# Optimization experiments

Hardware: AMD Instinct MI355X
Metric: run time of the kernel (lower is better)

Reference implementation:

```python
import jax, jax.numpy as jnp
import numpy as np

N_NODES = 500000


def gcn_conv(x, row, col, W, b, n_nodes):
    # x: [N, Fin]; row/col: [E+N] (self-loops already appended)
    h = x @ W                                      # [N, Fout]
    ones = jnp.ones(row.shape[0], dtype=h.dtype)
    deg = jax.ops.segment_sum(ones, col, num_segments=n_nodes)  # in-degree incl self-loop
    dis = jnp.where(deg > 0, jax.lax.rsqrt(deg), 0.0)
    norm = dis[row] * dis[col]                     # [E+N]
    msgs = norm[:, None] * h[row]                  # gather + scale, [E+N, Fout]
    out = jax.ops.segment_sum(msgs, col, num_segments=n_nodes)
    return out + b


def setup_inputs() -> dict:
    key = jax.random.key(0)
    k1, k2, k3, k4 = jax.random.split(key, 4)
    x = jax.random.normal(k1, (N_NODES, 3), dtype=jnp.float32)
    edge_index = jax.random.randint(k2, (2, 16000000), 0, N_NODES, dtype=jnp.int64)
    # glorot-style weights, zero bias (PyG GCNConv defaults)
    W1 = jax.random.normal(k3, (3, 16), dtype=jnp.float32) * (6.0 / (3 + 16)) ** 0.5
    b1 = jnp.zeros((16,), dtype=jnp.float32)
    W2 = jax.random.normal(k4, (16, 7), dtype=jnp.float32) * (6.0 / (16 + 7)) ** 0.5
    b2 = jnp.zeros((7,), dtype=jnp.float32)
    return {"x": x, "edge_index": edge_index, "W1": W1, "b1": b1, "W2": W2, "b2": b2}


def reference(x, edge_index, W1, b1, W2, b2):
    n = x.shape[0]
    loops = jnp.arange(n, dtype=edge_index.dtype)
    row = jnp.concatenate([edge_index[0], loops])  # sources
    col = jnp.concatenate([edge_index[1], loops])  # targets
    h = gcn_conv(x, row, col, W1, b1, n)
    h = jax.nn.relu(h)
    h = gcn_conv(h, row, col, W2, b2, n)
    return jax.nn.log_softmax(h, axis=1)
```

## Files before the change

### kernel.cpp

```cpp
#include <hip/hip_runtime.h>
#include <hip/hip_fp16.h>
#include <hip/hip_fp8.h>
#include <math.h>


#define BSH 9
#define BNODES 512
#define NBUK_MAX 1024
#define NKEY 1024
#define CAP 17408
#define PC 16384
#define HCAP 9216

typedef _Float16 half4v __attribute__((ext_vector_type(4)));
typedef unsigned char uchar8v __attribute__((ext_vector_type(8)));
typedef float float4v __attribute__((ext_vector_type(4)));
typedef unsigned int uint4v __attribute__((ext_vector_type(4)));

__device__ __forceinline__ float fp8_dec(unsigned char b) {
    __hip_fp8_e4m3 f;
    f.__x = (__hip_fp8_storage_t)b;
    return (float)f;
}

__global__ __launch_bounds__(512) void part_kernel(const int* __restrict__ row,
                                                   const int* __restrict__ col,
                                                   int* __restrict__ gCount,
                                                   unsigned int* __restrict__ packed,
                                                   int E, int nbuk) {
    __shared__ int lh[NBUK_MAX];
    __shared__ int lcnt[NBUK_MAX];
    __shared__ int gpos[NBUK_MAX];
    __shared__ int wsum[8];
    __shared__ unsigned int stage[PC];
    int tid = threadIdx.x;
    for (int i = tid; i < NBUK_MAX; i += 512) lh[i] = 0;
    __syncthreads();
    int base = blockIdx.x * PC;
    int emax = E - base; if (emax > PC) emax = PC;
    int e4 = emax >> 2;
    const uint4v* c4 = (const uint4v*)(col + base);
    const uint4v* r4 = (const uint4v*)(row + base);
    for (int i = tid; i < e4; i += 512) {
        uint4v u = c4[i];
        atomicAdd(&lh[u[0] >> BSH], 1);
        atomicAdd(&lh[u[1] >> BSH], 1);
        atomicAdd(&lh[u[2] >> BSH], 1);
        atomicAdd(&lh[u[3] >> BSH], 1);
    }
    for (int k = (e4 << 2) + tid; k < emax; k += 512)
        atomicAdd(&lh[(unsigned)col[base + k] >> BSH], 1);
    __syncthreads();
    int i0 = 2 * tid, i1 = 2 * tid + 1;
    int c0 = lh[i0], c1 = lh[i1];
    int lane = tid & 63, wv = tid >> 6;
    int v = c0 + c1;
    for (int off = 1; off < 64; off <<= 1) {
        int u = __shfl_up(v, off);
        if (lane >= off) v += u;
    }
    if (lane == 63) wsum[wv] = v;
    __syncthreads();
    if (tid < 64) {
        int w = (tid < 8) ? wsum[tid] : 0;
        for (int off = 1; off < 8; off <<= 1) {
            int u = __shfl_up(w, off);
            if (tid >= off) w += u;
        }
        if (tid < 8) wsum[tid] = w;
    }
    __syncthreads();
    int incl = (wv ? wsum[wv - 1] : 0) + v;
    int e1 = incl - c1;
    int e0 = e1 - c0;
    lh[i0] = e0; lh[i1] = e1;
    lcnt[i0] = c0; lcnt[i1] = c1;
    if (i0 < nbuk && c0 > 0) gpos[i0] = atomicAdd(&gCount[i0], c0);
    if (i1 < nbuk && c1 > 0) gpos[i1] = atomicAdd(&gCount[i1], c1);
    __syncthreads();
    for (int i = tid; i < e4; i += 512) {
        uint4v uc = __builtin_nontemporal_load(&c4[i]);
        uint4v ur = __builtin_nontemporal_load(&r4[i]);
        int p;
        p = atomicAdd(&lh[uc[0] >> BSH], 1);
        stage[p] = (ur[0] << BSH) | (uc[0] & (BNODES - 1));
        p = atomicAdd(&lh[uc[1] >> BSH], 1);
        stage[p] = (ur[1] << BSH) | (uc[1] & (BNODES - 1));
        p = atomicAdd(&lh[uc[2] >> BSH], 1);
        stage[p] = (ur[2] << BSH) | (uc[2] & (BNODES - 1));
        p = atomicAdd(&lh[uc[3] >> BSH], 1);
        stage[p] = (ur[3] << BSH) | (uc[3] & (BNODES - 1));
    }
    for (int k = (e4 << 2) + tid; k < emax; k += 512) {
        unsigned int c = (unsigned)__builtin_nontemporal_load(&col[base + k]);
        unsigned int r = (unsigned)__builtin_nontemporal_load(&row[base + k]);
        int p = atomicAdd(&lh[c >> BSH], 1);
        stage[p] = (r << BSH) | (c & (BNODES - 1));
    }
    __syncthreads();
    int grp = tid >> 4, gln = tid & 15;
    for (int b = grp; b < nbuk; b += 32) {
        int cnt = lcnt[b];
        if (cnt == 0) continue;
        int lo = lh[b] - cnt, gp = gpos[b];
        size_t outb = (size_t)b * CAP;
        for (int j = gln; j < cnt; j += 16) {
            int pos = gp + j;
            if (pos < CAP) packed[outb + pos] = stage[lo + j];
        }
    }
}

__global__ __launch_bounds__(512) void sort_kernel(unsigned int* __restrict__ packed,
                                                   const int* __restrict__ gCount,
                                                   const float* __restrict__ x,
                                                   float* __restrict__ dis,
                                                   half4v* __restrict__ xsH,
                                                   int* __restrict__ nS,
                                                   int* __restrict__ nM,
                                                   int* __restrict__ nH,
                                                   int* __restrict__ nE,
                                                   int* __restrict__ bLo,
                                                   int n, int half) {
    __shared__ int lcur[NKEY];
    __shared__ int kcnt[NKEY];
    __shared__ int wsum[8];
    __shared__ unsigned int stage[CAP];
    int tid = threadIdx.x;
    int b = blockIdx.x;
    size_t base = (size_t)b * CAP;
    int m = gCount[b];
    if (m > CAP) m = CAP;
    lcur[tid] = 0; lcur[tid + 512] = 0;
    __syncthreads();
    int m4 = m >> 2;
    const uint4v* p4c = (const uint4v*)(packed + base);
    for (int i = tid; i < m4; i += 512) {
        uint4v u = p4c[i];
        atomicAdd(&lcur[(((int)(u[0] >> BSH) >= half) << BSH) | (u[0] & (BNODES - 1))], 1);
        atomicAdd(&lcur[(((int)(u[1] >> BSH) >= half) << BSH) | (u[1] & (BNODES - 1))], 1);
        atomicAdd(&lcur[(((int)(u[2] >> BSH) >= half) << BSH) | (u[2] & (BNODES - 1))], 1);
        atomicAdd(&lcur[(((int)(u[3] >> BSH) >= half) << BSH) | (u[3] & (BNODES - 1))], 1);
    }
    for (int k = (m4 << 2) + tid; k < m; k += 512) {
        unsigned int u = packed[base + k];
        atomicAdd(&lcur[(((int)(u >> BSH) >= half) << BSH) | (u & (BNODES - 1))], 1);
    }
    __syncthreads();
    int i0 = 2 * tid, i1 = 2 * tid + 1;
    int c0 = lcur[i0], c1 = lcur[i1];
    int lane = tid & 63, wv = tid >> 6;
    int v = c0 + c1;
    for (int off = 1; off < 64; off <<= 1) {
        int u = __shfl_up(v, off);
        if (lane >= off) v += u;
    }
    if (lane == 63) wsum[wv] = v;
    __syncthreads();
    if (tid < 64) {
        int w = (tid < 8) ? wsum[tid] : 0;
        for (int off = 1; off < 8; off <<= 1) {
            int u = __shfl_up(w, off);
            if (tid >= off) w += u;
        }
        if (tid < 8) wsum[tid] = w;
    }
    __syncthreads();
    int incl = (wv ? wsum[wv - 1] : 0) + v;
    int e1 = incl - c1;
    int e0 = e1 - c0;
    lcur[i0] = e0; lcur[i1] = e1;
    kcnt[i0] = c0; kcnt[i1] = c1;
    __syncthreads();
    int node = (b << BSH) + tid;
    if (node < n) {
        int oLo = lcur[tid],       cLo = kcnt[tid];
        int oHi = lcur[512 + tid], cHi = kcnt[512 + tid];
        nS[node] = (int)base + oLo;
        nM[node] = (int)base + oLo + cLo;
        nH[node] = (int)base + oHi;
        nE[node] = (int)base + oHi + cHi;
        float d = rsqrtf((float)(cLo + cHi) + 1.0f);
        dis[node] = d;
        half4v h;
        h[0] = (_Float16)(d * x[3 * node]);
        h[1] = (_Float16)(d * x[3 * node + 1]);
        h[2] = (_Float16)(d * x[3 * node + 2]);
        h[3] = (_Float16)0.0f;
        xsH[node] = h;
    }
    if (tid == 0) bLo[b] = lcur[512];
    __syncthreads();
    for (int i = tid; i < m4; i += 512) {
        uint4v u = __builtin_nontemporal_load(&p4c[i]);
        int p;
        p = atomicAdd(&lcur[(((int)(u[0] >> BSH) >= half) << BSH) | (u[0] & (BNODES - 1))], 1);
        stage[p] = u[0] >> BSH;
        p = atomicAdd(&lcur[(((int)(u[1] >> BSH) >= half) << BSH) | (u[1] & (BNODES - 1))], 1);
        stage[p] = u[1] >> BSH;
        p = atomicAdd(&lcur[(((int)(u[2] >> BSH) >= half) << BSH) | (u[2] & (BNODES - 1))], 1);
        stage[p] = u[2] >> BSH;
        p = atomicAdd(&lcur[(((int)(u[3] >> BSH) >= half) << BSH) | (u[3] & (BNODES - 1))], 1);
        stage[p] = u[3] >> BSH;
    }
    for (int k = (m4 << 2) + tid; k < m; k += 512) {
        unsigned int u = __builtin_nontemporal_load(&packed[base + k]);
        int p = atomicAdd(&lcur[(((int)(u >> BSH) >= half) << BSH) | (u & (BNODES - 1))], 1);
        stage[p] = u >> BSH;
    }
    __syncthreads();
    uint4v* p4 = (uint4v*)(packed + base);
    const uint4v* s4 = (const uint4v*)stage;
    for (int i = tid; i < m4; i += 512) __builtin_nontemporal_store(s4[i], &p4[i]);
    for (int k = (m4 << 2) + tid; k < m; k += 512)
        __builtin_nontemporal_store(stage[k], &packed[base + k]);
}

__global__ __launch_bounds__(512) void l1_kernel(const int* __restrict__ nS, const int* __restrict__ nM,
                          const int* __restrict__ nH, const int* __restrict__ nE,
                          const unsigned int* __restrict__ packed,
                          const int* __restrict__ bLo, const int* __restrict__ gCount,
                          const float* __restrict__ dis, const half4v* __restrict__ xsH,
                          const float* __restrict__ W1, const float* __restrict__ b1,
                          const float* __restrict__ W2, uchar8v* __restrict__ hsB, int n) {
    __shared__ uint4v sidx4[HCAP / 4];
    __shared__ float sW1[48], sb1[16], sW2[112];
    unsigned int* sidx = (unsigned int*)sidx4;
    int tid = threadIdx.x, b = blockIdx.x;
    for (int t = tid; t < 48; t += 512) sW1[t] = W1[t];
    for (int t = tid; t < 16; t += 512) sb1[t] = b1[t];
    for (int t = tid; t < 112; t += 512) sW2[t] = W2[t];
    size_t base = (size_t)b * CAP;
    int m = gCount[b]; if (m > CAP) m = CAP;
    int lo = bLo[b];
    int node = (b << BSH) + tid;
    bool alive = node < n;
    int stagedL = lo < HCAP ? lo : HCAP;
    int st4 = stagedL >> 2;
    const uint4v* p4 = (const uint4v*)(packed + base);
    for (int i = tid; i < st4; i += 512) sidx4[i] = __builtin_nontemporal_load(&p4[i]);
    for (int k = (st4 << 2) + tid; k < stagedL; k += 512)
        sidx[k] = __builtin_nontemporal_load(&packed[base + k]);
    __syncthreads();
    float v0 = 0.0f, v1 = 0.0f, v2 = 0.0f;
    int s = 0, e = 0;
    if (alive) {
        s = __builtin_nontemporal_load(&nS[node]) - (int)base;
        e = __builtin_nontemporal_load(&nM[node]) - (int)base;
        half4v sv = xsH[node];
        v0 = (float)sv[0]; v1 = (float)sv[1]; v2 = (float)sv[2];
        int ke = e < stagedL ? e : stagedL;
        int k = s;
        for (; k + 4 <= ke; k += 4) {
            unsigned int r0 = sidx[k], r1 = sidx[k + 1], r2 = sidx[k + 2], r3 = sidx[k + 3];
            half4v a0 = xsH[r0], a1 = xsH[r1], a2 = xsH[r2], a3 = xsH[r3];
            v0 += (float)a0[0] + (float)a1[0] + (float)a2[0] + (float)a3[0];
            v1 += (float)a0[1] + (float)a1[1] + (float)a2[1] + (float)a3[1];
            v2 += (float)a0[2] + (float)a1[2] + (float)a2[2] + (float)a3[2];
        }
        for (; k < ke; k++) {
            half4v a = xsH[sidx[k]];
            v0 += (float)a[0]; v1 += (float)a[1]; v2 += (float)a[2];
        }
        for (; k < e; k++) {
            half4v a = xsH[__builtin_nontemporal_load(&packed[base + k])];
            v0 += (float)a[0]; v1 += (float)a[1]; v2 += (float)a[2];
        }
    }
    __syncthreads();
    int off0 = lo & 3;
    int astart = lo - off0;
    int hiw = m - astart;
    int stagedH = hiw < HCAP ? hiw : HCAP;
    st4 = stagedH >> 2;
    const uint4v* p4h = (const uint4v*)(packed + base + astart);
    for (int i = tid; i < st4; i += 512) sidx4[i] = __builtin_nontemporal_load(&p4h[i]);
    for (int k = (st4 << 2) + tid; k < stagedH; k += 512)
        sidx[k] = __builtin_nontemporal_load(&packed[base + astart + k]);
    __syncthreads();
    if (!alive) return;
    s = __builtin_nontemporal_load(&nH[node]) - (int)base;
    e = __builtin_nontemporal_load(&nE[node]) - (int)base;
    int glim = astart + stagedH;
    int ke = e < glim ? e : glim;
    int k = s;
    for (; k + 4 <= ke; k += 4) {
        int q = k - astart;
        unsigned int r0 = sidx[q], r1 = sidx[q + 1], r2 = sidx[q + 2], r3 = sidx[q + 3];
        half4v a0 = xsH[r0], a1 = xsH[r1], a2 = xsH[r2], a3 = xsH[r3];
        v0 += (float)a0[0] + (float)a1[0] + (float)a2[0] + (float)a3[0];
        v1 += (float)a0[1] + (float)a1[1] + (float)a2[1] + (float)a3[1];
        v2 += (float)a0[2] + (float)a1[2] + (float)a2[2] + (float)a3[2];
    }
    for (; k < ke; k++) {
        half4v a = xsH[sidx[k - astart]];
        v0 += (float)a[0]; v1 += (float)a[1]; v2 += (float)a[2];
    }
    for (; k < e; k++) {
        half4v a = xsH[__builtin_nontemporal_load(&packed[base + k])];
        v0 += (float)a[0]; v1 += (float)a[1]; v2 += (float)a[2];
    }
    float d = __builtin_nontemporal_load(&dis[node]);
    float h[16];
#pragma unroll
    for (int j = 0; j < 16; j++) {
        float t = v0 * sW1[j] + v1 * sW1[16 + j] + v2 * sW1[32 + j];
        h[j] = fmaxf(d * t + sb1[j], 0.0f);
    }
    uchar8v o;
#pragma unroll
    for (int t2 = 0; t2 < 7; t2++) {
        float s2 = 0.0f;
#pragma unroll
        for (int j = 0; j < 16; j++) s2 += h[j] * sW2[j * 7 + t2];
        o[t2] = (unsigned char)__hip_fp8_e4m3(d * s2).__x;
    }
    o[7] = 0;
    __builtin_nontemporal_store(o, &hsB[node]);
}

__global__ __launch_bounds__(512) void l2_kernel(const int* __restrict__ nS, const int* __restrict__ nM,
                          const int* __restrict__ nH, const int* __restrict__ nE,
                          const unsigned int* __restrict__ packed,
                          const int* __restrict__ bLo, const int* __restrict__ gCount,
                          const float* __restrict__ dis, const uchar8v* __restrict__ hsB,
                          const float* __restrict__ b2, float* __restrict__ out, int n) {
    __shared__ uint4v sidx4[HCAP / 4];
    unsigned int* sidx = (unsigned int*)sidx4;
    int tid = threadIdx.x, b = blockIdx.x;
    size_t base = (size_t)b * CAP;
    int m = gCount[b]; if (m > CAP) m = CAP;
    int lo = bLo[b];
    int node = (b << BSH) + tid;
    bool alive = node < n;
    int stagedL = lo < HCAP ? lo : HCAP;
    int st4 = stagedL >> 2;
    const uint4v* p4 = (const uint4v*)(packed + base);
    for (int i = tid; i < st4; i += 512) sidx4[i] = __builtin_nontemporal_load(&p4[i]);
    for (int k = (st4 << 2) + tid; k < stagedL; k += 512)
        sidx[k] = __builtin_nontemporal_load(&packed[base + k]);
    __syncthreads();
    float a[7] = {0, 0, 0, 0, 0, 0, 0};
    int s = 0, e = 0;
    if (alive) {
        s = __builtin_nontemporal_load(&nS[node]) - (int)base;
        e = __builtin_nontemporal_load(&nM[node]) - (int)base;
        uchar8v sv = hsB[node];
#pragma unroll
        for (int t = 0; t < 7; t++) a[t] = fp8_dec(sv[t]);
        int ke = e < stagedL ? e : stagedL;
        int k = s;
        for (; k + 4 <= ke; k += 4) {
            unsigned int r0 = sidx[k], r1 = sidx[k + 1], r2 = sidx[k + 2], r3 = sidx[k + 3];
            uchar8v p0 = hsB[r0], p1 = hsB[r1], p2 = hsB[r2], p3 = hsB[r3];
#pragma unroll
            for (int t = 0; t < 7; t++)
                a[t] += fp8_dec(p0[t]) + fp8_dec(p1[t]) + fp8_dec(p2[t]) + fp8_dec(p3[t]);
        }
        for (; k < ke; k++) {
            uchar8v p = hsB[sidx[k]];
#pragma unroll
            for (int t = 0; t < 7; t++) a[t] += fp8_dec(p[t]);
        }
        for (; k < e; k++) {
            uchar8v p = hsB[__builtin_nontemporal_load(&packed[base + k])];
#pragma unroll
            for (int t = 0; t < 7; t++) a[t] += fp8_dec(p[t]);
        }
    }
    __syncthreads();
    int off0 = lo & 3;
    int astart = lo - off0;
    int hiw = m - astart;
    int stagedH = hiw < HCAP ? hiw : HCAP;
    st4 = stagedH >> 2;
    const uint4v* p4h = (const uint4v*)(packed + base + astart);
    for (int i = tid; i < st4; i += 512) sidx4[i] = __builtin_nontemporal_load(&p4h[i]);
    for (int k = (st4 << 2) + tid; k < stagedH; k += 512)
        sidx[k] = __builtin_nontemporal_load(&packed[base + astart + k]);
    __syncthreads();
    if (!alive) return;
    s = __builtin_nontemporal_load(&nH[node]) - (int)base;
    e = __builtin_nontemporal_load(&nE[node]) - (int)base;
    int glim = astart + stagedH;
    int ke = e < glim ? e : glim;
    int k = s;
    for (; k + 4 <= ke; k += 4) {
        int q = k - astart;
        unsigned int r0 = sidx[q], r1 = sidx[q + 1], r2 = sidx[q + 2], r3 = sidx[q + 3];
        uchar8v p0 = hsB[r0], p1 = hsB[r1], p2 = hsB[r2], p3 = hsB[r3];
#pragma unroll
        for (int t = 0; t < 7; t++)
            a[t] += fp8_dec(p0[t]) + fp8_dec(p1[t]) + fp8_dec(p2[t]) + fp8_dec(p3[t]);
    }
    for (; k < ke; k++) {
        uchar8v p = hsB[sidx[k - astart]];
#pragma unroll
        for (int t = 0; t < 7; t++) a[t] += fp8_dec(p[t]);
    }
    for (; k < e; k++) {
        uchar8v p = hsB[__builtin_nontemporal_load(&packed[base + k])];
#pragma unroll
        for (int t = 0; t < 7; t++) a[t] += fp8_dec(p[t]);
    }
    float d = __builtin_nontemporal_load(&dis[node]);
    float o[7];
    float mm = -INFINITY;
#pragma unroll
    for (int t = 0; t < 7; t++) {
        o[t] = d * a[t] + b2[t];
        mm = fmaxf(mm, o[t]);
    }
    float ssum = 0.0f;
#pragma unroll
    for (int t = 0; t < 7; t++) ssum += expf(o[t] - mm);
    float lse = mm + logf(ssum);
    float* p = out + 7 * (size_t)node;
#pragma unroll
    for (int t = 0; t < 7; t++) __builtin_nontemporal_store(o[t] - lse, &p[t]);
}

extern "C" void kernel_launch(void* const* d_in, const int* in_sizes, int n_in,
                              void* d_out, int out_size, void* d_ws, size_t ws_size,
                              hipStream_t stream) {
    const float* x  = (const float*)d_in[0];
    const int*   ei = (const int*)d_in[1];
    const float* W1 = (const float*)d_in[2];
    const float* b1 = (const float*)d_in[3];
    const float* W2 = (const float*)d_in[4];
    const float* b2 = (const float*)d_in[5];

    const int n = in_sizes[0] / 3;
    const int E = in_sizes[1] / 2;
    const int* row = ei;
    const int* col = ei + E;
    const int nbuk = (n + BNODES - 1) >> BSH;
    const int half = n / 2;

    char* ws = (char*)d_ws;
    size_t off = 0;
    unsigned int* packed = (unsigned int*)(ws + off); off += (size_t)nbuk * CAP * 4;
    half4v*  xsH = (half4v*)(ws + off);  off += (size_t)n * 8;
    uchar8v* hsB = (uchar8v*)(ws + off); off += (size_t)n * 8;
    float* dis = (float*)(ws + off); off += (size_t)n * 4;
    int* nS  = (int*)(ws + off); off += (size_t)n * 4;
    int* nM  = (int*)(ws + off); off += (size_t)n * 4;
    int* nH  = (int*)(ws + off); off += (size_t)n * 4;
    int* nE  = (int*)(ws + off); off += (size_t)n * 4;
    int* gCount = (int*)(ws + off); off += (size_t)nbuk * 4;
    int* bLo    = (int*)(ws + off); off += (size_t)nbuk * 4;

    hipMemsetAsync(gCount, 0, (size_t)nbuk * 4, stream);

    const int gbP = (E + PC - 1) / PC;

    part_kernel<<<gbP, 512, 0, stream>>>(row, col, gCount, packed, E, nbuk);
    sort_kernel<<<nbuk, 512, 0, stream>>>(packed, gCount, x, dis, xsH, nS, nM, nH, nE, bLo, n, half);
    l1_kernel<<<nbuk, 512, 0, stream>>>(nS, nM, nH, nE, packed, bLo, gCount, dis, xsH, W1, b1, W2, hsB, n);
    l2_kernel<<<nbuk, 512, 0, stream>>>(nS, nM, nH, nE, packed, bLo, gCount, dis, hsB, b2, (float*)d_out, n);
}
```

Before: 457.7 us.

## Switch aggregation to edge-balanced segmented reduction with shared-memory atomics

The layer kernels no longer give each thread one destination node and its variable-length edge list. Each thread now takes an equal contiguous chunk of the sorted edge list, runs a segmented sum over runs of the same local target, and flushes partial sums into per-block shared-memory accumulators with atomics. The sort therefore keeps the full packed word, including the local target bits, and the per-node offset arrays nS/nM/nH/nE are dropped. This aims to remove load imbalance from skewed degrees and the offset-array traffic. In exchange it adds shared-memory float atomics, a padded index staging layout (HCAP reduced to fit), and a non-deterministic summation order.

```diff
diff --git a/kernel.cpp b/kernel.cpp
--- a/kernel.cpp
+++ b/kernel.cpp
@@ -10,11 +10,11 @@
 #define NKEY 1024
 #define CAP 17408
 #define PC 16384
-#define HCAP 9216
+#define HCAP 8960
+#define HPADW (HCAP + (HCAP >> 5))
 
 typedef _Float16 half4v __attribute__((ext_vector_type(4)));
 typedef unsigned char uchar8v __attribute__((ext_vector_type(8)));
-typedef float float4v __attribute__((ext_vector_type(4)));
 typedef unsigned int uint4v __attribute__((ext_vector_type(4)));
 
 __device__ __forceinline__ float fp8_dec(unsigned char b) {
@@ -103,11 +103,11 @@
         int cnt = lcnt[b];
         if (cnt == 0) continue;
         int lo = lh[b] - cnt, gp = gpos[b];
-        size_t outb = (size_t)b * CAP;
-        for (int j = gln; j < cnt; j += 16) {
-            int pos = gp + j;
-            if (pos < CAP) packed[outb + pos] = stage[lo + j];
-        }
+        int lim = cnt;
+        if (gp + lim > CAP) lim = CAP - gp;
+        size_t outb = (size_t)b * CAP + gp;
+        for (int j = gln; j < lim; j += 16)
+            packed[outb + j] = stage[lo + j];
     }
 }
 
@@ -116,10 +116,6 @@
                                                    const float* __restrict__ x,
                                                    float* __restrict__ dis,
                                                    half4v* __restrict__ xsH,
-                                                   int* __restrict__ nS,
-                                                   int* __restrict__ nM,
-                                                   int* __restrict__ nH,
-                                                   int* __restrict__ nE,
                                                    int* __restrict__ bLo,
                                                    int n, int half) {
     __shared__ int lcur[NKEY];
@@ -174,12 +170,8 @@
     __syncthreads();
     int node = (b << BSH) + tid;
     if (node < n) {
-        int oLo = lcur[tid],       cLo = kcnt[tid];
-        int oHi = lcur[512 + tid], cHi = kcnt[512 + tid];
-        nS[node] = (int)base + oLo;
-        nM[node] = (int)base + oLo + cLo;
-        nH[node] = (int)base + oHi;
-        nE[node] = (int)base + oHi + cHi;
+        int cLo = kcnt[tid];
+        int cHi = kcnt[512 + tid];
         float d = rsqrtf((float)(cLo + cHi) + 1.0f);
         dis[node] = d;
         half4v h;
@@ -195,18 +187,18 @@
         uint4v u = __builtin_nontemporal_load(&p4c[i]);
         int p;
         p = atomicAdd(&lcur[(((int)(u[0] >> BSH) >= half) << BSH) | (u[0] & (BNODES - 1))], 1);
-        stage[p] = u[0] >> BSH;
+        stage[p] = u[0];
         p = atomicAdd(&lcur[(((int)(u[1] >> BSH) >= half) << BSH) | (u[1] & (BNODES - 1))], 1);
-        stage[p] = u[1] >> BSH;
+        stage[p] = u[1];
         p = atomicAdd(&lcur[(((int)(u[2] >> BSH) >= half) << BSH) | (u[2] & (BNODES - 1))], 1);
-        stage[p] = u[2] >> BSH;
+        stage[p] = u[2];
         p = atomicAdd(&lcur[(((int)(u[3] >> BSH) >= half) << BSH) | (u[3] & (BNODES - 1))], 1);
-        stage[p] = u[3] >> BSH;
+        stage[p] = u[3];
     }
     for (int k = (m4 << 2) + tid; k < m; k += 512) {
         unsigned int u = __builtin_nontemporal_load(&packed[base + k]);
         int p = atomicAdd(&lcur[(((int)(u >> BSH) >= half) << BSH) | (u & (BNODES - 1))], 1);
-        stage[p] = u >> BSH;
+        stage[p] = u;
     }
     __syncthreads();
     uint4v* p4 = (uint4v*)(packed + base);
@@ -216,91 +208,62 @@
         __builtin_nontemporal_store(stage[k], &packed[base + k]);
 }
 
-__global__ __launch_bounds__(512) void l1_kernel(const int* __restrict__ nS, const int* __restrict__ nM,
-                          const int* __restrict__ nH, const int* __restrict__ nE,
-                          const unsigned int* __restrict__ packed,
-                          const int* __restrict__ bLo, const int* __restrict__ gCount,
+__global__ __launch_bounds__(512) void l1_kernel(const unsigned int* __restrict__ packed,
+                          const int* __restrict__ gCount, const int* __restrict__ bLo,
                           const float* __restrict__ dis, const half4v* __restrict__ xsH,
                           const float* __restrict__ W1, const float* __restrict__ b1,
                           const float* __restrict__ W2, uchar8v* __restrict__ hsB, int n) {
-    __shared__ uint4v sidx4[HCAP / 4];
+    __shared__ unsigned int sidx[HPADW];
+    __shared__ float aX[BNODES], aY[BNODES], aZ[BNODES];
     __shared__ float sW1[48], sb1[16], sW2[112];
-    unsigned int* sidx = (unsigned int*)sidx4;
     int tid = threadIdx.x, b = blockIdx.x;
     for (int t = tid; t < 48; t += 512) sW1[t] = W1[t];
     for (int t = tid; t < 16; t += 512) sb1[t] = b1[t];
     for (int t = tid; t < 112; t += 512) sW2[t] = W2[t];
-    size_t base = (size_t)b * CAP;
+    aX[tid] = 0.0f; aY[tid] = 0.0f; aZ[tid] = 0.0f;
+    size_t bb = (size_t)b * CAP;
     int m = gCount[b]; if (m > CAP) m = CAP;
     int lo = bLo[b];
+#pragma unroll
+    for (int ph = 0; ph < 2; ph++) {
+        int beg = ph ? lo : 0;
+        int end = ph ? m : lo;
+        int cnt = end - beg;
+        int staged = cnt < HCAP ? cnt : HCAP;
+        __syncthreads();
+        for (int k = tid; k < staged; k += 512)
+            sidx[k + (k >> 5)] = __builtin_nontemporal_load(&packed[bb + beg + k]);
+        __syncthreads();
+        int chunk = (cnt + 511) >> 9;
+        int ks = tid * chunk;
+        int ke = ks + chunk; if (ke > cnt) ke = cnt;
+        float x0 = 0.0f, x1 = 0.0f, x2 = 0.0f;
+        int cur = -1;
+        for (int k = ks; k < ke; k++) {
+            unsigned int u = (k < staged) ? sidx[k + (k >> 5)]
+                                          : __builtin_nontemporal_load(&packed[bb + beg + k]);
+            int lc = u & (BNODES - 1);
+            if (lc != cur) {
+                if (cur >= 0) {
+                    atomicAdd(&aX[cur], x0); atomicAdd(&aY[cur], x1); atomicAdd(&aZ[cur], x2);
+                }
+                cur = lc; x0 = 0.0f; x1 = 0.0f; x2 = 0.0f;
+            }
+            half4v a = xsH[u >> BSH];
+            x0 += (float)a[0]; x1 += (float)a[1]; x2 += (float)a[2];
+        }
+        if (cur >= 0) {
+            atomicAdd(&aX[cur], x0); atomicAdd(&aY[cur], x1); atomicAdd(&aZ[cur], x2);
+        }
+    }
+    __syncthreads();
     int node = (b << BSH) + tid;
-    bool alive = node < n;
-    int stagedL = lo < HCAP ? lo : HCAP;
-    int st4 = stagedL >> 2;
-    const uint4v* p4 = (const uint4v*)(packed + base);
-    for (int i = tid; i < st4; i += 512) sidx4[i] = __builtin_nontemporal_load(&p4[i]);
-    for (int k = (st4 << 2) + tid; k < stagedL; k += 512)
-        sidx[k] = __builtin_nontemporal_load(&packed[base + k]);
-    __syncthreads();
-    float v0 = 0.0f, v1 = 0.0f, v2 = 0.0f;
-    int s = 0, e = 0;
-    if (alive) {
-        s = __builtin_nontemporal_load(&nS[node]) - (int)base;
-        e = __builtin_nontemporal_load(&nM[node]) - (int)base;
-        half4v sv = xsH[node];
-        v0 = (float)sv[0]; v1 = (float)sv[1]; v2 = (float)sv[2];
-        int ke = e < stagedL ? e : stagedL;
-        int k = s;
-        for (; k + 4 <= ke; k += 4) {
-            unsigned int r0 = sidx[k], r1 = sidx[k + 1], r2 = sidx[k + 2], r3 = sidx[k + 3];
-            half4v a0 = xsH[r0], a1 = xsH[r1], a2 = xsH[r2], a3 = xsH[r3];
-            v0 += (float)a0[0] + (float)a1[0] + (float)a2[0] + (float)a3[0];
-            v1 += (float)a0[1] + (float)a1[1] + (float)a2[1] + (float)a3[1];
-            v2 += (float)a0[2] + (float)a1[2] + (float)a2[2] + (float)a3[2];
-        }
-        for (; k < ke; k++) {
-            half4v a = xsH[sidx[k]];
-            v0 += (float)a[0]; v1 += (float)a[1]; v2 += (float)a[2];
-        }
-        for (; k < e; k++) {
-            half4v a = xsH[__builtin_nontemporal_load(&packed[base + k])];
-            v0 += (float)a[0]; v1 += (float)a[1]; v2 += (float)a[2];
-        }
-    }
-    __syncthreads();
-    int off0 = lo & 3;
-    int astart = lo - off0;
-    int hiw = m - astart;
-    int stagedH = hiw < HCAP ? hiw : HCAP;
-    st4 = stagedH >> 2;
-    const uint4v* p4h = (const uint4v*)(packed + base + astart);
-    for (int i = tid; i < st4; i += 512) sidx4[i] = __builtin_nontemporal_load(&p4h[i]);
-    for (int k = (st4 << 2) + tid; k < stagedH; k += 512)
-        sidx[k] = __builtin_nontemporal_load(&packed[base + astart + k]);
-    __syncthreads();
-    if (!alive) return;
-    s = __builtin_nontemporal_load(&nH[node]) - (int)base;
-    e = __builtin_nontemporal_load(&nE[node]) - (int)base;
-    int glim = astart + stagedH;
-    int ke = e < glim ? e : glim;
-    int k = s;
-    for (; k + 4 <= ke; k += 4) {
-        int q = k - astart;
-        unsigned int r0 = sidx[q], r1 = sidx[q + 1], r2 = sidx[q + 2], r3 = sidx[q + 3];
-        half4v a0 = xsH[r0], a1 = xsH[r1], a2 = xsH[r2], a3 = xsH[r3];
-        v0 += (float)a0[0] + (float)a1[0] + (float)a2[0] + (float)a3[0];
-        v1 += (float)a0[1] + (float)a1[1] + (float)a2[1] + (float)a3[1];
-        v2 += (float)a0[2] + (float)a1[2] + (float)a2[2] + (float)a3[2];
-    }
-    for (; k < ke; k++) {
-        half4v a = xsH[sidx[k - astart]];
-        v0 += (float)a[0]; v1 += (float)a[1]; v2 += (float)a[2];
-    }
-    for (; k < e; k++) {
-        half4v a = xsH[__builtin_nontemporal_load(&packed[base + k])];
-        v0 += (float)a[0]; v1 += (float)a[1]; v2 += (float)a[2];
-    }
-    float d = __builtin_nontemporal_load(&dis[node]);
+    if (node >= n) return;
+    half4v sv = xsH[node];
+    float v0 = aX[tid] + (float)sv[0];
+    float v1 = aY[tid] + (float)sv[1];
+    float v2 = aZ[tid] + (float)sv[2];
+    float d = dis[node];
     float h[16];
 #pragma unroll
     for (int j = 0; j < 16; j++) {
@@ -319,96 +282,66 @@
     __builtin_nontemporal_store(o, &hsB[node]);
 }
 
-__global__ __launch_bounds__(512) void l2_kernel(const int* __restrict__ nS, const int* __restrict__ nM,
-                          const int* __restrict__ nH, const int* __restrict__ nE,
-                          const unsigned int* __restrict__ packed,
-                          const int* __restrict__ bLo, const int* __restrict__ gCount,
+__global__ __launch_bounds__(512) void l2_kernel(const unsigned int* __restrict__ packed,
+                          const int* __restrict__ gCount, const int* __restrict__ bLo,
                           const float* __restrict__ dis, const uchar8v* __restrict__ hsB,
                           const float* __restrict__ b2, float* __restrict__ out, int n) {
-    __shared__ uint4v sidx4[HCAP / 4];
-    unsigned int* sidx = (unsigned int*)sidx4;
+    __shared__ unsigned int sidx[HPADW];
+    __shared__ float A[7][BNODES];
     int tid = threadIdx.x, b = blockIdx.x;
-    size_t base = (size_t)b * CAP;
+#pragma unroll
+    for (int t = 0; t < 7; t++) A[t][tid] = 0.0f;
+    size_t bb = (size_t)b * CAP;
     int m = gCount[b]; if (m > CAP) m = CAP;
     int lo = bLo[b];
+#pragma unroll
+    for (int ph = 0; ph < 2; ph++) {
+        int beg = ph ? lo : 0;
+        int end = ph ? m : lo;
+        int cnt = end - beg;
+        int staged = cnt < HCAP ? cnt : HCAP;
+        __syncthreads();
+        for (int k = tid; k < staged; k += 512)
+            sidx[k + (k >> 5)] = __builtin_nontemporal_load(&packed[bb + beg + k]);
+        __syncthreads();
+        int chunk = (cnt + 511) >> 9;
+        int ks = tid * chunk;
+        int ke = ks + chunk; if (ke > cnt) ke = cnt;
+        float ac[7] = {0, 0, 0, 0, 0, 0, 0};
+        int cur = -1;
+        for (int k = ks; k < ke; k++) {
+            unsigned int u = (k < staged) ? sidx[k + (k >> 5)]
+                                          : __builtin_nontemporal_load(&packed[bb + beg + k]);
+            int lc = u & (BNODES - 1);
+            if (lc != cur) {
+                if (cur >= 0) {
+#pragma unroll
+                    for (int t = 0; t < 7; t++) atomicAdd(&A[t][cur], ac[t]);
+                }
+                cur = lc;
+#pragma unroll
+                for (int t = 0; t < 7; t++) ac[t] = 0.0f;
+            }
+            uchar8v p = hsB[u >> BSH];
+#pragma unroll
+            for (int t = 0; t < 7; t++) ac[t] += fp8_dec(p[t]);
+        }
+        if (cur >= 0) {
+#pragma unroll
+            for (int t = 0; t < 7; t++) atomicAdd(&A[t][cur], ac[t]);
+        }
+    }
+    __syncthreads();
     int node = (b << BSH) + tid;
-    bool alive = node < n;
-    int stagedL = lo < HCAP ? lo : HCAP;
-    int st4 = stagedL >> 2;
-    const uint4v* p4 = (const uint4v*)(packed + base);
-    for (int i = tid; i < st4; i += 512) sidx4[i] = __builtin_nontemporal_load(&p4[i]);
-    for (int k = (st4 << 2) + tid; k < stagedL; k += 512)
-        sidx[k] = __builtin_nontemporal_load(&packed[base + k]);
-    __syncthreads();
-    float a[7] = {0, 0, 0, 0, 0, 0, 0};
-    int s = 0, e = 0;
-    if (alive) {
-        s = __builtin_nontemporal_load(&nS[node]) - (int)base;
-        e = __builtin_nontemporal_load(&nM[node]) - (int)base;
-        uchar8v sv = hsB[node];
-#pragma unroll
-        for (int t = 0; t < 7; t++) a[t] = fp8_dec(sv[t]);
-        int ke = e < stagedL ? e : stagedL;
-        int k = s;
-        for (; k + 4 <= ke; k += 4) {
-            unsigned int r0 = sidx[k], r1 = sidx[k + 1], r2 = sidx[k + 2], r3 = sidx[k + 3];
-            uchar8v p0 = hsB[r0], p1 = hsB[r1], p2 = hsB[r2], p3 = hsB[r3];
-#pragma unroll
-            for (int t = 0; t < 7; t++)
-                a[t] += fp8_dec(p0[t]) + fp8_dec(p1[t]) + fp8_dec(p2[t]) + fp8_dec(p3[t]);
-        }
-        for (; k < ke; k++) {
-            uchar8v p = hsB[sidx[k]];
-#pragma unroll
-            for (int t = 0; t < 7; t++) a[t] += fp8_dec(p[t]);
-        }
-        for (; k < e; k++) {
-            uchar8v p = hsB[__builtin_nontemporal_load(&packed[base + k])];
-#pragma unroll
-            for (int t = 0; t < 7; t++) a[t] += fp8_dec(p[t]);
-        }
-    }
-    __syncthreads();
-    int off0 = lo & 3;
-    int astart = lo - off0;
-    int hiw = m - astart;
-    int stagedH = hiw < HCAP ? hiw : HCAP;
-    st4 = stagedH >> 2;
-    const uint4v* p4h = (const uint4v*)(packed + base + astart);
-    for (int i = tid; i < st4; i += 512) sidx4[i] = __builtin_nontemporal_load(&p4h[i]);
-    for (int k = (st4 << 2) + tid; k < stagedH; k += 512)
-        sidx[k] = __builtin_nontemporal_load(&packed[base + astart + k]);
-    __syncthreads();
-    if (!alive) return;
-    s = __builtin_nontemporal_load(&nH[node]) - (int)base;
-    e = __builtin_nontemporal_load(&nE[node]) - (int)base;
-    int glim = astart + stagedH;
-    int ke = e < glim ? e : glim;
-    int k = s;
-    for (; k + 4 <= ke; k += 4) {
-        int q = k - astart;
-        unsigned int r0 = sidx[q], r1 = sidx[q + 1], r2 = sidx[q + 2], r3 = sidx[q + 3];
-        uchar8v p0 = hsB[r0], p1 = hsB[r1], p2 = hsB[r2], p3 = hsB[r3];
-#pragma unroll
-        for (int t = 0; t < 7; t++)
-            a[t] += fp8_dec(p0[t]) + fp8_dec(p1[t]) + fp8_dec(p2[t]) + fp8_dec(p3[t]);
-    }
-    for (; k < ke; k++) {
-        uchar8v p = hsB[sidx[k - astart]];
-#pragma unroll
-        for (int t = 0; t < 7; t++) a[t] += fp8_dec(p[t]);
-    }
-    for (; k < e; k++) {
-        uchar8v p = hsB[__builtin_nontemporal_load(&packed[base + k])];
-#pragma unroll
-        for (int t = 0; t < 7; t++) a[t] += fp8_dec(p[t]);
-    }
-    float d = __builtin_nontemporal_load(&dis[node]);
+    if (node >= n) return;
+    uchar8v sv = hsB[node];
+    float d = dis[node];
     float o[7];
     float mm = -INFINITY;
 #pragma unroll
     for (int t = 0; t < 7; t++) {
-        o[t] = d * a[t] + b2[t];
+        float a = A[t][tid] + fp8_dec(sv[t]);
+        o[t] = d * a + b2[t];
         mm = fmaxf(mm, o[t]);
     }
     float ssum = 0.0f;
@@ -443,10 +376,6 @@
     half4v*  xsH = (half4v*)(ws + off);  off += (size_t)n * 8;
     uchar8v* hsB = (uchar8v*)(ws + off); off += (size_t)n * 8;
     float* dis = (float*)(ws + off); off += (size_t)n * 4;
-    int* nS  = (int*)(ws + off); off += (size_t)n * 4;
-    int* nM  = (int*)(ws + off); off += (size_t)n * 4;
-    int* nH  = (int*)(ws + off); off += (size_t)n * 4;
-    int* nE  = (int*)(ws + off); off += (size_t)n * 4;
     int* gCount = (int*)(ws + off); off += (size_t)nbuk * 4;
     int* bLo    = (int*)(ws + off); off += (size_t)nbuk * 4;
 
@@ -455,7 +384,7 @@
     const int gbP = (E + PC - 1) / PC;
 
     part_kernel<<<gbP, 512, 0, stream>>>(row, col, gCount, packed, E, nbuk);
-    sort_kernel<<<nbuk, 512, 0, stream>>>(packed, gCount, x, dis, xsH, nS, nM, nH, nE, bLo, n, half);
-    l1_kernel<<<nbuk, 512, 0, stream>>>(nS, nM, nH, nE, packed, bLo, gCount, dis, xsH, W1, b1, W2, hsB, n);
-    l2_kernel<<<nbuk, 512, 0, stream>>>(nS, nM, nH, nE, packed, bLo, gCount, dis, hsB, b2, (float*)d_out, n);
-}
+    sort_kernel<<<nbuk, 512, 0, stream>>>(packed, gCount, x, dis, xsH, bLo, n, half);
+    l1_kernel<<<nbuk, 512, 0, stream>>>(packed, gCount, bLo, dis, xsH, W1, b1, W2, hsB, n);
+    l2_kernel<<<nbuk, 512, 0, stream>>>(packed, gCount, bLo, dis, hsB, b2, (float*)d_out, n);
+}
```

Result: slower. 518.6 us (+13.3%).
